# Kernel optimization log

Measured on AMD Instinct MI355X. Metric: run time of the kernel, lower is better.

The kernel has to match this reference:

```python
import jax, jax.numpy as jnp
import numpy as np

N_HEAD = 16


def setup_inputs() -> dict:
    key = jax.random.key(0)
    ks = jax.random.split(key, 5)
    B, T, C = 4, 2048, 1024
    s = 0.02
    x = jax.random.normal(ks[0], (B, T, C), jnp.float32)
    wq = jax.random.normal(ks[1], (C, C), jnp.float32) * s
    wk = jax.random.normal(ks[2], (C, C), jnp.float32) * s
    wv = jax.random.normal(ks[3], (C, C), jnp.float32) * s
    wp = jax.random.normal(ks[4], (C, C), jnp.float32) * s
    zb = jnp.zeros((C,), jnp.float32)
    return {"x": x, "wq": wq, "bq": zb, "wk": wk, "bk": zb,
            "wv": wv, "bv": zb, "wp": wp, "bp": zb}


def _rope_cos_sin(T, D):
    half = D // 2
    i = jnp.arange(half, dtype=jnp.float32)
    alpha = 1.0 / (10000.0 ** (2.0 * i / D))        # [half]
    ang = jnp.arange(T, dtype=jnp.float32)[:, None] * alpha  # [T, half]
    return jnp.cos(ang), jnp.sin(ang)


def _apply_rope(t, cos, sin):
    # t: [B, H, T, D]; non-interleaved halves as in the torch module
    half = t.shape[-1] // 2
    xr, xi = t[..., :half], t[..., half:]
    return jnp.concatenate([xr * cos - xi * sin, xr * sin + xi * cos], axis=-1)


def reference(x, wq, bq, wk, bk, wv, bv, wp, bp):
    B, T, C = x.shape
    H = N_HEAD
    D = C // H
    # QKV projections (torch Linear: x @ W.T + b)
    def heads(w, b):
        return (x @ w.T + b).reshape(B, T, H, D).transpose(0, 2, 1, 3)
    q, k, v = heads(wq, bq), heads(wk, bk), heads(wv, bv)
    cos, sin = _rope_cos_sin(T, D)  # each [T, D//2], broadcasts over B,H
    q = _apply_rope(q, cos, sin)
    k = _apply_rope(k, cos, sin)
    scale = 1.0 / np.sqrt(D).astype(np.float32)
    att = jnp.einsum('bhtd,bhsd->bhts', q, k) * scale  # [B,H,T,T]
    causal = jnp.tril(jnp.ones((T, T), bool))
    att = jnp.where(causal, att, jnp.float32(-jnp.inf))
    att = jax.nn.softmax(att, axis=-1)
    y = jnp.einsum('bhts,bhsd->bhtd', att, v)  # [B,H,T,D]
    y = y.transpose(0, 2, 1, 3).reshape(B, T, C)
    return y @ wp.T + bp
```

## Files before the change

### kernel.cpp

```cpp
#include <hip/hip_runtime.h>
#include <math.h>

constexpr int B = 4, T = 2048, C = 1024, H = 16, D = 64;
constexpr int M = B * T;
constexpr size_t BTC = (size_t)B * T * C;
constexpr float QSCALE = 0.18033688011112042f;
constexpr float ROPE_C = -0.415241011861f;

typedef short bf16x8 __attribute__((ext_vector_type(8)));
typedef float f32x4 __attribute__((ext_vector_type(4)));

__device__ inline ushort f2bf(float f) {
  union { float f; unsigned u; } cv; cv.f = f;
  unsigned u = cv.u;
  u += 0x7fffu + ((u >> 16) & 1u);
  return (ushort)(u >> 16);
}
__device__ inline ushort f2bfr(float f) {
  union { float f; unsigned u; } cv; cv.f = f;
  return (ushort)((cv.u + 0x8000u) >> 16);
}

__device__ inline void async_load16(const void* g, void* l) {
  __builtin_amdgcn_global_load_lds(
      (const __attribute__((address_space(1))) void*)g,
      (__attribute__((address_space(3))) void*)l, 16, 0, 0);
}

__device__ __forceinline__ bf16x8 ones_frag() {
  bf16x8 v;
#pragma unroll
  for (int i = 0; i < 8; i++) v[i] = (short)0x3F80;
  return v;
}

__global__ __launch_bounds__(256) void f32_to_bf16(
    const float* __restrict__ in, ushort* __restrict__ outp) {
  int i = (blockIdx.x * 256 + threadIdx.x) * 4;
  float4 v = *(const float4*)(in + i);
  ushort4 o;
  o.x = f2bf(v.x); o.y = f2bf(v.y); o.z = f2bf(v.z); o.w = f2bf(v.w);
  *(ushort4*)(outp + i) = o;
}

__global__ __launch_bounds__(256) void conv_weights(
    const float* __restrict__ w0, const float* __restrict__ w1,
    const float* __restrict__ w2, const float* __restrict__ w3,
    ushort* __restrict__ outp) {
  const int seg_blocks = (C * C) / 1024;
  int seg = blockIdx.x / seg_blocks;
  int blk = blockIdx.x - seg * seg_blocks;
  const float* src = (seg == 0) ? w0 : (seg == 1) ? w1 : (seg == 2) ? w2 : w3;
  int i = (blk * 256 + threadIdx.x) * 4;
  float4 v = *(const float4*)(src + i);
  ushort4 o;
  o.x = f2bf(v.x); o.y = f2bf(v.y); o.z = f2bf(v.z); o.w = f2bf(v.w);
  *(ushort4*)(outp + (size_t)seg * C * C + i) = o;
}

constexpr int QNT = C / 64;

__global__ __launch_bounds__(512, 2) void gemm_qkv_256x128(
    const ushort* __restrict__ A, const ushort* __restrict__ Wt,
    const float* __restrict__ b0, const float* __restrict__ b1,
    const float* __restrict__ b2, ushort* __restrict__ outq,
    ushort* __restrict__ outk, ushort* __restrict__ outv) {
  __shared__ ushort As[2][256 * 64] __attribute__((aligned(16)));
  __shared__ ushort Bs[3][128 * 64] __attribute__((aligned(16)));
  const int tid = threadIdx.x;
  const int lane = tid & 63;
  const int lrow = lane & 15, quad = lane >> 4;
  const int wave = tid >> 6;
  const int wr = wave >> 1, wc = wave & 1;
  const int x7 = lrow & 7;

  int bid = blockIdx.y * 24 + blockIdx.x;
  int lin = (bid & 7) * 96 + (bid >> 3);
  int row0 = (lin / 24) * 256;
  int col0 = (lin % 24) * 128;

  unsigned gaA[4], gaB[2];
#pragma unroll
  for (int i = 0; i < 4; i++) {
    int c = tid + i * 512;
    int r = c >> 3, cl = c & 7;
    gaA[i] = (unsigned)(row0 + r) * C + (cl ^ (r & 7)) * 8;
  }
#pragma unroll
  for (int i = 0; i < 2; i++) {
    int c = tid + i * 512;
    int r = c >> 3, cl = c & 7;
    gaB[i] = (unsigned)(col0 + r) * C + (cl ^ (r & 7)) * 8;
  }

  f32x4 acc[4][4];
#pragma unroll
  for (int i = 0; i < 4; i++)
#pragma unroll
    for (int j = 0; j < 4; j++) acc[i][j] = (f32x4){0.f, 0.f, 0.f, 0.f};

#pragma unroll
  for (int i = 0; i < 4; i++)
    async_load16(A + gaA[i], &As[0][(tid + i * 512) * 8]);
#pragma unroll
  for (int i = 0; i < 2; i++)
    async_load16(Wt + gaB[i], &Bs[0][(tid + i * 512) * 8]);
#pragma unroll
  for (int i = 0; i < 2; i++)
    async_load16(Wt + gaB[i] + 64, &Bs[1][(tid + i * 512) * 8]);
  asm volatile("s_waitcnt vmcnt(2)" ::: "memory");
  __builtin_amdgcn_sched_barrier(0);
  __builtin_amdgcn_s_barrier();

  int bi = 0;
  for (int t = 0; t < QNT; ++t) {
    const int pa = t & 1;
    const ushort* Ap = As[pa];
    const ushort* Bp = Bs[bi];

    {
      const int slot = (quad ^ x7) * 8;
      bf16x8 af[4], bfr[4];
#pragma unroll
      for (int i = 0; i < 4; i++)
        af[i] = *(const bf16x8*)&Ap[(wr * 64 + i * 16 + lrow) * 64 + slot];
#pragma unroll
      for (int j = 0; j < 4; j++)
        bfr[j] = *(const bf16x8*)&Bp[(wc * 64 + j * 16 + lrow) * 64 + slot];
      if (t + 1 < QNT) {
#pragma unroll
        for (int i = 0; i < 4; i++)
          async_load16(A + gaA[i] + (t + 1) * 64,
                       &As[pa ^ 1][(tid + i * 512) * 8]);
      }
      __builtin_amdgcn_s_barrier();
      asm volatile("s_waitcnt lgkmcnt(0)" ::: "memory");
      __builtin_amdgcn_sched_barrier(0);
      __builtin_amdgcn_s_setprio(1);
#pragma unroll
      for (int i = 0; i < 4; i++)
#pragma unroll
        for (int j = 0; j < 4; j++)
          acc[i][j] = __builtin_amdgcn_mfma_f32_16x16x32_bf16(
              af[i], bfr[j], acc[i][j], 0, 0, 0);
      __builtin_amdgcn_s_setprio(0);
      __builtin_amdgcn_s_barrier();
    }

    {
      const int slot = ((4 + quad) ^ x7) * 8;
      bf16x8 af[4], bfr[4];
#pragma unroll
      for (int i = 0; i < 4; i++)
        af[i] = *(const bf16x8*)&Ap[(wr * 64 + i * 16 + lrow) * 64 + slot];
#pragma unroll
      for (int j = 0; j < 4; j++)
        bfr[j] = *(const bf16x8*)&Bp[(wc * 64 + j * 16 + lrow) * 64 + slot];
      if (t + 2 < QNT) {
        int bi2 = bi - 1; if (bi2 < 0) bi2 = 2;
#pragma unroll
        for (int i = 0; i < 2; i++)
          async_load16(Wt + gaB[i] + (t + 2) * 64,
                       &Bs[bi2][(tid + i * 512) * 8]);
      }
      __builtin_amdgcn_s_barrier();
      asm volatile("s_waitcnt lgkmcnt(0)" ::: "memory");
      __builtin_amdgcn_sched_barrier(0);
      __builtin_amdgcn_s_setprio(1);
#pragma unroll
      for (int i = 0; i < 4; i++)
#pragma unroll
        for (int j = 0; j < 4; j++)
          acc[i][j] = __builtin_amdgcn_mfma_f32_16x16x32_bf16(
              af[i], bfr[j], acc[i][j], 0, 0, 0);
      __builtin_amdgcn_s_setprio(0);
      if (t + 2 < QNT) {
        asm volatile("s_waitcnt vmcnt(2)" ::: "memory");
      } else {
        asm volatile("s_waitcnt vmcnt(0)" ::: "memory");
      }
      __builtin_amdgcn_sched_barrier(0);
      __builtin_amdgcn_s_barrier();
    }
    bi = (bi + 1 == 3) ? 0 : bi + 1;
  }

  const int nb = col0 + wc * 64;
  const int mbase = row0 + wr * 64;
  const float* bias = (col0 < 1024) ? b0 : (col0 < 2048) ? b1 : b2;
  float bn[4];
#pragma unroll
  for (int j = 0; j < 4; j++) bn[j] = bias[(nb & 1023) + j * 16 + lrow];

  int seg = nb >> 10;
  int hh = (nb & 1023) >> 6;
  if (seg < 2) {
    ushort* dst = (seg == 0) ? outq : outk;
    float scale = (seg == 0) ? QSCALE : 1.0f;
    float a0 = __builtin_amdgcn_exp2f((float)lrow * ROPE_C);
    float a1 = __builtin_amdgcn_exp2f((float)(lrow + 16) * ROPE_C);
#pragma unroll
    for (int i = 0; i < 4; i++) {
#pragma unroll
      for (int r = 0; r < 4; r++) {
        int m = mbase + i * 16 + quad * 4 + r;
        int tt = m & (T - 1), bb = m >> 11;
        float s0, c0, s1, c1;
        __sincosf((float)tt * a0, &s0, &c0);
        __sincosf((float)tt * a1, &s1, &c1);
        float xr0 = acc[i][0][r] + bn[0];
        float xi0 = acc[i][2][r] + bn[2];
        float xr1 = acc[i][1][r] + bn[1];
        float xi1 = acc[i][3][r] + bn[3];
        ushort* pp = dst + ((size_t)(bb * H + hh) * T + tt) * D + lrow;
        pp[0]  = f2bf((xr0 * c0 - xi0 * s0) * scale);
        pp[32] = f2bf((xr0 * s0 + xi0 * c0) * scale);
        pp[16] = f2bf((xr1 * c1 - xi1 * s1) * scale);
        pp[48] = f2bf((xr1 * s1 + xi1 * c1) * scale);
      }
    }
  } else {
#pragma unroll
    for (int i = 0; i < 4; i++) {
      int m0 = mbase + i * 16 + quad * 4;
      int t0 = m0 & (T - 1), bb = m0 >> 11;
      size_t base = (size_t)(bb * H + hh) * D * T + t0;
#pragma unroll
      for (int j = 0; j < 4; j++) {
        int d = j * 16 + lrow;
        ushort4 pk;
        pk.x = f2bf(acc[i][j][0] + bn[j]);
        pk.y = f2bf(acc[i][j][1] + bn[j]);
        pk.z = f2bf(acc[i][j][2] + bn[j]);
        pk.w = f2bf(acc[i][j][3] + bn[j]);
        *(ushort4*)(outv + base + (size_t)d * T) = pk;
      }
    }
  }
}

#define GT 128
#define GBK 64
template <int OM>
__global__ __launch_bounds__(256) void gemm_mfma_bt(
    const ushort* __restrict__ A, const ushort* __restrict__ Wt,
    const float* __restrict__ b0, const float* __restrict__ b1,
    const float* __restrict__ b2, void* __restrict__ out1,
    void* __restrict__ out2, void* __restrict__ out3,
    int N, int K) {
  __shared__ ushort As[GT * GBK] __attribute__((aligned(16)));
  __shared__ ushort Bs[GT * GBK] __attribute__((aligned(16)));
  int tid = threadIdx.x;
  int lane = tid & 63;
  int lrow = lane & 15, quad = lane >> 4;
  int wave = tid >> 6;
  int wr = wave >> 1, wc = wave & 1;
  int row0 = blockIdx.y * GT;
  int col0 = blockIdx.x * GT;
  const float* bias = (col0 < 1024) ? b0 : (col0 < 2048) ? b1 : b2;

  size_t ga[4], gb[4];
#pragma unroll
  for (int i = 0; i < 4; i++) {
    int cc = tid + i * 256;
    int r = cc >> 3, cl = cc & 7;
    int g = (cl ^ (r & 7)) * 8;
    ga[i] = (size_t)(row0 + r) * K + g;
    gb[i] = (size_t)(col0 + r) * K + g;
  }
  int x7 = lrow & 7;

  f32x4 acc[4][4];
#pragma unroll
  for (int i = 0; i < 4; i++)
#pragma unroll
    for (int j = 0; j < 4; j++) acc[i][j] = (f32x4){0.f, 0.f, 0.f, 0.f};

  for (int k0 = 0; k0 < K; k0 += GBK) {
#pragma unroll
    for (int i = 0; i < 4; i++) {
      int cc = tid + i * 256;
      async_load16(A + ga[i] + k0, &As[cc * 8]);
      async_load16(Wt + gb[i] + k0, &Bs[cc * 8]);
    }
    __syncthreads();
#pragma unroll
    for (int kh = 0; kh < 2; kh++) {
      int slot = ((kh * 4 + quad) ^ x7) * 8;
      bf16x8 af[4], bfr[4];
#pragma unroll
      for (int i = 0; i < 4; i++)
        af[i] = *(const bf16x8*)&As[(wr * 64 + i * 16 + lrow) * GBK + slot];
#pragma unroll
      for (int j = 0; j < 4; j++)
        bfr[j] = *(const bf16x8*)&Bs[(wc * 64 + j * 16 + lrow) * GBK + slot];
#pragma unroll
      for (int i = 0; i < 4; i++)
#pragma unroll
        for (int j = 0; j < 4; j++)
          acc[i][j] = __builtin_amdgcn_mfma_f32_16x16x32_bf16(af[i], bfr[j], acc[i][j], 0, 0, 0);
    }
    __syncthreads();
  }

  int nb = col0 + wc * 64;
  int mbase = row0 + wr * 64;
  float bn[4];
#pragma unroll
  for (int j = 0; j < 4; j++) bn[j] = bias[(nb & 1023) + j * 16 + lrow];

  if (OM == 0) {
    float* outp = (float*)out1;
#pragma unroll
    for (int i = 0; i < 4; i++)
#pragma unroll
      for (int j = 0; j < 4; j++) {
        int n = nb + j * 16 + lrow;
#pragma unroll
        for (int r = 0; r < 4; r++) {
          int m = mbase + i * 16 + quad * 4 + r;
          outp[(size_t)m * N + n] = acc[i][j][r] + bn[j];
        }
      }
  }
}

__device__ __forceinline__ void stage_kv(
    const ushort* kbh, const ushort* vbh, int s0,
    ushort* Kl, ushort* Vl, int tid) {
#pragma unroll
  for (int i = 0; i < 2; i++) {
    int c = tid + i * 256;
    int r = c >> 3, cc = c & 7;
    int g = (cc ^ (r & 7)) * 8;
    async_load16(kbh + (size_t)(s0 + r) * D + g, Kl + c * 8);
    async_load16(vbh + (size_t)r * T + s0 + g, Vl + c * 8);
  }
}

template <int MODE>
__device__ __forceinline__ void attn_step4(
    int s0, const ushort* KL, const ushort* VL, ushort* P,
    const bf16x8 (&qf)[2][2], int lrow, int quad, int sw0, int sw1,
    int qg0, int qg1, f32x4 (&o)[4][2], f32x4 (&ol)[2]) {
  bf16x8 kf0[4], kf1[4];
#pragma unroll
  for (int kt = 0; kt < 4; kt++) {
    int base = (kt * 16 + lrow) * 64;
    kf0[kt] = *(const bf16x8*)&KL[base + sw0];
    kf1[kt] = *(const bf16x8*)&KL[base + sw1];
  }
  bf16x8 vf0[4], vf1[4];
#pragma unroll
  for (int ds = 0; ds < 4; ds++) {
    int base = (ds * 16 + lrow) * 64;
    vf0[ds] = *(const bf16x8*)&VL[base + sw0];
    vf1[ds] = *(const bf16x8*)&VL[base + sw1];
  }
#pragma unroll
  for (int g = 0; g < 2; g++) {
    if (MODE == 2 && g == 0) continue;
    int qg = g ? qg1 : qg0;
    f32x4 st[4];
#pragma unroll
    for (int kt = 0; kt < 4; kt++) {
      f32x4 z = {0.f, 0.f, 0.f, 0.f};
      st[kt] = __builtin_amdgcn_mfma_f32_16x16x32_bf16(kf0[kt], qf[g][0], z, 0, 0, 0);
      st[kt] = __builtin_amdgcn_mfma_f32_16x16x32_bf16(kf1[kt], qf[g][1], st[kt], 0, 0, 0);
    }
    if ((MODE == 1 && g == 0) || (MODE == 2 && g == 1)) {
#pragma unroll
      for (int kt = 0; kt < 4; kt++)
#pragma unroll
        for (int r = 0; r < 4; r++)
          if (s0 + kt * 16 + quad * 4 + r > qg) st[kt][r] = -1e30f;
    }
#pragma unroll
    for (int kt = 0; kt < 4; kt++) {
      ushort4 pk;
      pk.x = f2bfr(__builtin_amdgcn_exp2f(st[kt][0]));
      pk.y = f2bfr(__builtin_amdgcn_exp2f(st[kt][1]));
      pk.z = f2bfr(__builtin_amdgcn_exp2f(st[kt][2]));
      pk.w = f2bfr(__builtin_amdgcn_exp2f(st[kt][3]));
      *(ushort4*)&P[((2 * kt + (quad >> 1)) * 32 + g * 16 + lrow) * 8 + (quad & 1) * 4] = pk;
    }
  }
  asm volatile("" ::: "memory");
  bf16x8 ones = ones_frag();
#pragma unroll
  for (int g = 0; g < 2; g++) {
    if (MODE == 2 && g == 0) continue;
    bf16x8 pf0 = *(const bf16x8*)&P[(quad * 32 + g * 16 + lrow) * 8];
    bf16x8 pf1 = *(const bf16x8*)&P[((quad + 4) * 32 + g * 16 + lrow) * 8];
    ol[g] = __builtin_amdgcn_mfma_f32_16x16x32_bf16(ones, pf0, ol[g], 0, 0, 0);
    ol[g] = __builtin_amdgcn_mfma_f32_16x16x32_bf16(ones, pf1, ol[g], 0, 0, 0);
#pragma unroll
    for (int ds = 0; ds < 4; ds++) {
      o[ds][g] = __builtin_amdgcn_mfma_f32_16x16x32_bf16(vf0[ds], pf0, o[ds][g], 0, 0, 0);
      o[ds][g] = __builtin_amdgcn_mfma_f32_16x16x32_bf16(vf1[ds], pf1, o[ds][g], 0, 0, 0);
    }
  }
}

__global__ __launch_bounds__(256, 3) void attn_mfma4(
    const ushort* __restrict__ qb_, const ushort* __restrict__ kb_,
    const ushort* __restrict__ vtb_, ushort* __restrict__ y) {
  __shared__ ushort Kl[2][64 * 64] __attribute__((aligned(16)));
  __shared__ ushort Vl[2][64 * 64] __attribute__((aligned(16)));
  __shared__ ushort Pl[4][2048] __attribute__((aligned(16)));
  int tid = threadIdx.x;
  int wave = tid >> 6, lane = tid & 63;
  int lrow = lane & 15, quad = lane >> 4;
  int qbi = 15 - (int)(blockIdx.x >> 6);
  int bh = blockIdx.x & 63;
  int b = bh >> 4, h = bh & 15;
  int Q0 = qbi * 128;
  ushort* P = Pl[wave];
  const ushort* kbh = kb_ + (size_t)bh * T * D;
  const ushort* vbh = vtb_ + (size_t)bh * D * T;

  int qg0 = Q0 + wave * 16 + lrow;
  int qg1 = qg0 + 64;
  bf16x8 qf[2][2];
  {
    const ushort* qp0 = qb_ + ((size_t)bh * T + qg0) * D + quad * 8;
    qf[0][0] = *(const bf16x8*)qp0;
    qf[0][1] = *(const bf16x8*)(qp0 + 32);
    const ushort* qp1 = qb_ + ((size_t)bh * T + qg1) * D + quad * 8;
    qf[1][0] = *(const bf16x8*)qp1;
    qf[1][1] = *(const bf16x8*)(qp1 + 32);
  }
  int r7 = lrow & 7;
  int sw0 = (quad ^ r7) * 8;
  int sw1 = ((quad + 4) ^ r7) * 8;

  f32x4 o[4][2];
#pragma unroll
  for (int ds = 0; ds < 4; ds++)
#pragma unroll
    for (int g = 0; g < 2; g++) o[ds][g] = (f32x4){0.f, 0.f, 0.f, 0.f};
  f32x4 ol[2] = {(f32x4){0.f, 0.f, 0.f, 0.f}, (f32x4){0.f, 0.f, 0.f, 0.f}};

  int trips = 2 * qbi + 2;
  stage_kv(kbh, vbh, 0, Kl[0], Vl[0], tid);
  int it = 0;
  for (; it < trips - 2; ++it) {
    __syncthreads();
    stage_kv(kbh, vbh, (it + 1) * 64, Kl[(it + 1) & 1], Vl[(it + 1) & 1], tid);
    attn_step4<0>(it * 64, Kl[it & 1], Vl[it & 1], P, qf, lrow, quad, sw0, sw1,
                  qg0, qg1, o, ol);
  }
  __syncthreads();
  stage_kv(kbh, vbh, (it + 1) * 64, Kl[(it + 1) & 1], Vl[(it + 1) & 1], tid);
  attn_step4<1>(it * 64, Kl[it & 1], Vl[it & 1], P, qf, lrow, quad, sw0, sw1,
                qg0, qg1, o, ol);
  ++it;
  __syncthreads();
  attn_step4<2>(it * 64, Kl[it & 1], Vl[it & 1], P, qf, lrow, quad, sw0, sw1,
                qg0, qg1, o, ol);

#pragma unroll
  for (int g = 0; g < 2; g++) {
    float inv = 1.f / ol[g][0];
    int qg = g ? qg1 : qg0;
#pragma unroll
    for (int ds = 0; ds < 4; ds++) {
      ushort4 pk;
      pk.x = f2bf(o[ds][g][0] * inv);
      pk.y = f2bf(o[ds][g][1] * inv);
      pk.z = f2bf(o[ds][g][2] * inv);
      pk.w = f2bf(o[ds][g][3] * inv);
      *(ushort4*)(y + ((size_t)b * T + qg) * C + h * D + ds * 16 + quad * 4) = pk;
    }
  }
}

extern "C" void kernel_launch(void* const* d_in, const int* in_sizes, int n_in,
                              void* d_out, int out_size, void* d_ws, size_t ws_size,
                              hipStream_t stream) {
  const float* x  = (const float*)d_in[0];
  const float* wq = (const float*)d_in[1];
  const float* bq = (const float*)d_in[2];
  const float* wk = (const float*)d_in[3];
  const float* bk = (const float*)d_in[4];
  const float* wv = (const float*)d_in[5];
  const float* bv = (const float*)d_in[6];
  const float* wp = (const float*)d_in[7];
  const float* bp = (const float*)d_in[8];
  float* out = (float*)d_out;

  ushort* xb    = (ushort*)d_ws;
  ushort* qb    = xb + BTC;
  ushort* kb    = qb + BTC;
  ushort* vtb   = kb + BTC;
  ushort* yb    = vtb + BTC;
  ushort* wqkvb = yb + BTC;
  ushort* wpb   = wqkvb + (size_t)3 * C * C;

  f32_to_bf16<<<(int)(BTC / 1024), 256, 0, stream>>>(x, xb);
  conv_weights<<<4 * (C * C) / 1024, 256, 0, stream>>>(wq, wk, wv, wp, wqkvb);

  dim3 qkv_grid(3 * C / 128, M / 256);
  gemm_qkv_256x128<<<qkv_grid, 512, 0, stream>>>(
      xb, wqkvb, bq, bk, bv, qb, kb, vtb);

  attn_mfma4<<<(B * H * T / 128), 256, 0, stream>>>(qb, kb, vtb, yb);

  dim3 proj_grid(C / GT, M / GT);
  gemm_mfma_bt<0><<<proj_grid, 256, 0, stream>>>(
      yb, wpb, bp, bp, bp, out, nullptr, nullptr, C, C);
}
```

Before: 247.2 us.

## Generalize pipelined 256x128 GEMM, use it for projection, drop intra-step barriers

Turns the triple-buffered, software-pipelined QKV GEMM into a template that takes an output mode and a column-tile count. The output projection now uses it in place of the simpler 128x128 kernel, which synchronised twice per K step and had no load/compute overlap. The main loop also drops the per-half barriers and explicit lgkmcnt waits, keeping a single vmcnt wait plus barrier per K iteration. This is meant to cut barrier stalls and hide global-load latency in both GEMMs. In exchange it relies on the single end-of-iteration barrier and compiler-inserted LDS waits for correctness, and the projection launch now uses larger 512-thread tiles, so there are fewer blocks.

Measured after the change: 231.5 us. -6.4%, faster.

```diff
diff --git a/kernel.cpp b/kernel.cpp
--- a/kernel.cpp
+++ b/kernel.cpp
@@ -60,11 +60,12 @@
 
 constexpr int QNT = C / 64;
 
-__global__ __launch_bounds__(512, 2) void gemm_qkv_256x128(
+template <int OM, int NCT>
+__global__ __launch_bounds__(512, 2) void gemm_pipe(
     const ushort* __restrict__ A, const ushort* __restrict__ Wt,
     const float* __restrict__ b0, const float* __restrict__ b1,
-    const float* __restrict__ b2, ushort* __restrict__ outq,
-    ushort* __restrict__ outk, ushort* __restrict__ outv) {
+    const float* __restrict__ b2, void* __restrict__ out1,
+    void* __restrict__ out2, void* __restrict__ out3) {
   __shared__ ushort As[2][256 * 64] __attribute__((aligned(16)));
   __shared__ ushort Bs[3][128 * 64] __attribute__((aligned(16)));
   const int tid = threadIdx.x;
@@ -74,10 +75,11 @@
   const int wr = wave >> 1, wc = wave & 1;
   const int x7 = lrow & 7;
 
-  int bid = blockIdx.y * 24 + blockIdx.x;
-  int lin = (bid & 7) * 96 + (bid >> 3);
-  int row0 = (lin / 24) * 256;
-  int col0 = (lin % 24) * 128;
+  int bid = blockIdx.y * NCT + blockIdx.x;
+  const int cpx = NCT * 4;
+  int lin = (bid & 7) * cpx + (bid >> 3);
+  int row0 = (lin / NCT) * 256;
+  int col0 = (lin % NCT) * 128;
 
   unsigned gaA[4], gaB[2];
 #pragma unroll
@@ -117,72 +119,66 @@
     const int pa = t & 1;
     const ushort* Ap = As[pa];
     const ushort* Bp = Bs[bi];
+    int bi2 = bi - 1; if (bi2 < 0) bi2 = 2;
 
     {
       const int slot = (quad ^ x7) * 8;
-      bf16x8 af[4], bfr[4];
+      bf16x8 aF[4], bF[4];
 #pragma unroll
       for (int i = 0; i < 4; i++)
-        af[i] = *(const bf16x8*)&Ap[(wr * 64 + i * 16 + lrow) * 64 + slot];
+        aF[i] = *(const bf16x8*)&Ap[(wr * 64 + i * 16 + lrow) * 64 + slot];
 #pragma unroll
       for (int j = 0; j < 4; j++)
-        bfr[j] = *(const bf16x8*)&Bp[(wc * 64 + j * 16 + lrow) * 64 + slot];
+        bF[j] = *(const bf16x8*)&Bp[(wc * 64 + j * 16 + lrow) * 64 + slot];
       if (t + 1 < QNT) {
 #pragma unroll
         for (int i = 0; i < 4; i++)
           async_load16(A + gaA[i] + (t + 1) * 64,
                        &As[pa ^ 1][(tid + i * 512) * 8]);
       }
-      __builtin_amdgcn_s_barrier();
-      asm volatile("s_waitcnt lgkmcnt(0)" ::: "memory");
-      __builtin_amdgcn_sched_barrier(0);
       __builtin_amdgcn_s_setprio(1);
 #pragma unroll
       for (int i = 0; i < 4; i++)
 #pragma unroll
         for (int j = 0; j < 4; j++)
           acc[i][j] = __builtin_amdgcn_mfma_f32_16x16x32_bf16(
-              af[i], bfr[j], acc[i][j], 0, 0, 0);
+              aF[i], bF[j], acc[i][j], 0, 0, 0);
       __builtin_amdgcn_s_setprio(0);
-      __builtin_amdgcn_s_barrier();
     }
 
     {
       const int slot = ((4 + quad) ^ x7) * 8;
-      bf16x8 af[4], bfr[4];
+      bf16x8 aF[4], bF[4];
 #pragma unroll
       for (int i = 0; i < 4; i++)
-        af[i] = *(const bf16x8*)&Ap[(wr * 64 + i * 16 + lrow) * 64 + slot];
+        aF[i] = *(const bf16x8*)&Ap[(wr * 64 + i * 16 + lrow) * 64 + slot];
 #pragma unroll
       for (int j = 0; j < 4; j++)
-        bfr[j] = *(const bf16x8*)&Bp[(wc * 64 + j * 16 + lrow) * 64 + slot];
+        bF[j] = *(const bf16x8*)&Bp[(wc * 64 + j * 16 + lrow) * 64 + slot];
       if (t + 2 < QNT) {
-        int bi2 = bi - 1; if (bi2 < 0) bi2 = 2;
 #pragma unroll
         for (int i = 0; i < 2; i++)
           async_load16(Wt + gaB[i] + (t + 2) * 64,
                        &Bs[bi2][(tid + i * 512) * 8]);
       }
-      __builtin_amdgcn_s_barrier();
-      asm volatile("s_waitcnt lgkmcnt(0)" ::: "memory");
-      __builtin_amdgcn_sched_barrier(0);
       __builtin_amdgcn_s_setprio(1);
 #pragma unroll
       for (int i = 0; i < 4; i++)
 #pragma unroll
         for (int j = 0; j < 4; j++)
           acc[i][j] = __builtin_amdgcn_mfma_f32_16x16x32_bf16(
-              af[i], bfr[j], acc[i][j], 0, 0, 0);
+              aF[i], bF[j], acc[i][j], 0, 0, 0);
       __builtin_amdgcn_s_setprio(0);
-      if (t + 2 < QNT) {
-        asm volatile("s_waitcnt vmcnt(2)" ::: "memory");
-      } else {
-        asm volatile("s_waitcnt vmcnt(0)" ::: "memory");
-      }
-      __builtin_amdgcn_sched_barrier(0);
-      __builtin_amdgcn_s_barrier();
-    }
-    bi = (bi + 1 == 3) ? 0 : bi + 1;
+    }
+
+    if (t + 2 < QNT) {
+      asm volatile("s_waitcnt vmcnt(2)" ::: "memory");
+    } else {
+      asm volatile("s_waitcnt vmcnt(0)" ::: "memory");
+    }
+    __builtin_amdgcn_sched_barrier(0);
+    __builtin_amdgcn_s_barrier();
+    bi = (bi == 2) ? 0 : bi + 1;
   }
 
   const int nb = col0 + wc * 64;
@@ -192,124 +188,8 @@
 #pragma unroll
   for (int j = 0; j < 4; j++) bn[j] = bias[(nb & 1023) + j * 16 + lrow];
 
-  int seg = nb >> 10;
-  int hh = (nb & 1023) >> 6;
-  if (seg < 2) {
-    ushort* dst = (seg == 0) ? outq : outk;
-    float scale = (seg == 0) ? QSCALE : 1.0f;
-    float a0 = __builtin_amdgcn_exp2f((float)lrow * ROPE_C);
-    float a1 = __builtin_amdgcn_exp2f((float)(lrow + 16) * ROPE_C);
-#pragma unroll
-    for (int i = 0; i < 4; i++) {
-#pragma unroll
-      for (int r = 0; r < 4; r++) {
-        int m = mbase + i * 16 + quad * 4 + r;
-        int tt = m & (T - 1), bb = m >> 11;
-        float s0, c0, s1, c1;
-        __sincosf((float)tt * a0, &s0, &c0);
-        __sincosf((float)tt * a1, &s1, &c1);
-        float xr0 = acc[i][0][r] + bn[0];
-        float xi0 = acc[i][2][r] + bn[2];
-        float xr1 = acc[i][1][r] + bn[1];
-        float xi1 = acc[i][3][r] + bn[3];
-        ushort* pp = dst + ((size_t)(bb * H + hh) * T + tt) * D + lrow;
-        pp[0]  = f2bf((xr0 * c0 - xi0 * s0) * scale);
-        pp[32] = f2bf((xr0 * s0 + xi0 * c0) * scale);
-        pp[16] = f2bf((xr1 * c1 - xi1 * s1) * scale);
-        pp[48] = f2bf((xr1 * s1 + xi1 * c1) * scale);
-      }
-    }
-  } else {
-#pragma unroll
-    for (int i = 0; i < 4; i++) {
-      int m0 = mbase + i * 16 + quad * 4;
-      int t0 = m0 & (T - 1), bb = m0 >> 11;
-      size_t base = (size_t)(bb * H + hh) * D * T + t0;
-#pragma unroll
-      for (int j = 0; j < 4; j++) {
-        int d = j * 16 + lrow;
-        ushort4 pk;
-        pk.x = f2bf(acc[i][j][0] + bn[j]);
-        pk.y = f2bf(acc[i][j][1] + bn[j]);
-        pk.z = f2bf(acc[i][j][2] + bn[j]);
-        pk.w = f2bf(acc[i][j][3] + bn[j]);
-        *(ushort4*)(outv + base + (size_t)d * T) = pk;
-      }
-    }
-  }
-}
-
-#define GT 128
-#define GBK 64
-template <int OM>
-__global__ __launch_bounds__(256) void gemm_mfma_bt(
-    const ushort* __restrict__ A, const ushort* __restrict__ Wt,
-    const float* __restrict__ b0, const float* __restrict__ b1,
-    const float* __restrict__ b2, void* __restrict__ out1,
-    void* __restrict__ out2, void* __restrict__ out3,
-    int N, int K) {
-  __shared__ ushort As[GT * GBK] __attribute__((aligned(16)));
-  __shared__ ushort Bs[GT * GBK] __attribute__((aligned(16)));
-  int tid = threadIdx.x;
-  int lane = tid & 63;
-  int lrow = lane & 15, quad = lane >> 4;
-  int wave = tid >> 6;
-  int wr = wave >> 1, wc = wave & 1;
-  int row0 = blockIdx.y * GT;
-  int col0 = blockIdx.x * GT;
-  const float* bias = (col0 < 1024) ? b0 : (col0 < 2048) ? b1 : b2;
-
-  size_t ga[4], gb[4];
-#pragma unroll
-  for (int i = 0; i < 4; i++) {
-    int cc = tid + i * 256;
-    int r = cc >> 3, cl = cc & 7;
-    int g = (cl ^ (r & 7)) * 8;
-    ga[i] = (size_t)(row0 + r) * K + g;
-    gb[i] = (size_t)(col0 + r) * K + g;
-  }
-  int x7 = lrow & 7;
-
-  f32x4 acc[4][4];
-#pragma unroll
-  for (int i = 0; i < 4; i++)
-#pragma unroll
-    for (int j = 0; j < 4; j++) acc[i][j] = (f32x4){0.f, 0.f, 0.f, 0.f};
-
-  for (int k0 = 0; k0 < K; k0 += GBK) {
-#pragma unroll
-    for (int i = 0; i < 4; i++) {
-      int cc = tid + i * 256;
-      async_load16(A + ga[i] + k0, &As[cc * 8]);
-      async_load16(Wt + gb[i] + k0, &Bs[cc * 8]);
-    }
-    __syncthreads();
-#pragma unroll
-    for (int kh = 0; kh < 2; kh++) {
-      int slot = ((kh * 4 + quad) ^ x7) * 8;
-      bf16x8 af[4], bfr[4];
-#pragma unroll
-      for (int i = 0; i < 4; i++)
-        af[i] = *(const bf16x8*)&As[(wr * 64 + i * 16 + lrow) * GBK + slot];
-#pragma unroll
-      for (int j = 0; j < 4; j++)
-        bfr[j] = *(const bf16x8*)&Bs[(wc * 64 + j * 16 + lrow) * GBK + slot];
-#pragma unroll
-      for (int i = 0; i < 4; i++)
-#pragma unroll
-        for (int j = 0; j < 4; j++)
-          acc[i][j] = __builtin_amdgcn_mfma_f32_16x16x32_bf16(af[i], bfr[j], acc[i][j], 0, 0, 0);
-    }
-    __syncthreads();
-  }
-
-  int nb = col0 + wc * 64;
-  int mbase = row0 + wr * 64;
-  float bn[4];
-#pragma unroll
-  for (int j = 0; j < 4; j++) bn[j] = bias[(nb & 1023) + j * 16 + lrow];
-
   if (OM == 0) {
+    const int N = NCT * 128;
     float* outp = (float*)out1;
 #pragma unroll
     for (int i = 0; i < 4; i++)
@@ -322,6 +202,53 @@
           outp[(size_t)m * N + n] = acc[i][j][r] + bn[j];
         }
       }
+  } else {
+    int seg = nb >> 10;
+    int hh = (nb & 1023) >> 6;
+    if (seg < 2) {
+      ushort* dst = (seg == 0) ? (ushort*)out1 : (ushort*)out2;
+      float scale = (seg == 0) ? QSCALE : 1.0f;
+      float a0 = __builtin_amdgcn_exp2f((float)lrow * ROPE_C);
+      float a1 = __builtin_amdgcn_exp2f((float)(lrow + 16) * ROPE_C);
+#pragma unroll
+      for (int i = 0; i < 4; i++) {
+#pragma unroll
+        for (int r = 0; r < 4; r++) {
+          int m = mbase + i * 16 + quad * 4 + r;
+          int tt = m & (T - 1), bb = m >> 11;
+          float s0, c0, s1, c1;
+          __sincosf((float)tt * a0, &s0, &c0);
+          __sincosf((float)tt * a1, &s1, &c1);
+          float xr0 = acc[i][0][r] + bn[0];
+          float xi0 = acc[i][2][r] + bn[2];
+          float xr1 = acc[i][1][r] + bn[1];
+          float xi1 = acc[i][3][r] + bn[3];
+          ushort* pp = dst + ((size_t)(bb * H + hh) * T + tt) * D + lrow;
+          pp[0]  = f2bf((xr0 * c0 - xi0 * s0) * scale);
+          pp[32] = f2bf((xr0 * s0 + xi0 * c0) * scale);
+          pp[16] = f2bf((xr1 * c1 - xi1 * s1) * scale);
+          pp[48] = f2bf((xr1 * s1 + xi1 * c1) * scale);
+        }
+      }
+    } else {
+      ushort* dst = (ushort*)out3;
+#pragma unroll
+      for (int i = 0; i < 4; i++) {
+        int m0 = mbase + i * 16 + quad * 4;
+        int t0 = m0 & (T - 1), bb = m0 >> 11;
+        size_t base = (size_t)(bb * H + hh) * D * T + t0;
+#pragma unroll
+        for (int j = 0; j < 4; j++) {
+          int d = j * 16 + lrow;
+          ushort4 pk;
+          pk.x = f2bf(acc[i][j][0] + bn[j]);
+          pk.y = f2bf(acc[i][j][1] + bn[j]);
+          pk.z = f2bf(acc[i][j][2] + bn[j]);
+          pk.w = f2bf(acc[i][j][3] + bn[j]);
+          *(ushort4*)(dst + base + (size_t)d * T) = pk;
+        }
+      }
+    }
   }
 }
 
@@ -501,12 +428,12 @@
   conv_weights<<<4 * (C * C) / 1024, 256, 0, stream>>>(wq, wk, wv, wp, wqkvb);
 
   dim3 qkv_grid(3 * C / 128, M / 256);
-  gemm_qkv_256x128<<<qkv_grid, 512, 0, stream>>>(
+  gemm_pipe<1, 24><<<qkv_grid, 512, 0, stream>>>(
       xb, wqkvb, bq, bk, bv, qb, kb, vtb);
 
   attn_mfma4<<<(B * H * T / 128), 256, 0, stream>>>(qb, kb, vtb, yb);
 
-  dim3 proj_grid(C / GT, M / GT);
-  gemm_mfma_bt<0><<<proj_grid, 256, 0, stream>>>(
-      yb, wpb, bp, bp, bp, out, nullptr, nullptr, C, C);
-}
+  dim3 proj_grid(C / 128, M / 256);
+  gemm_pipe<0, 8><<<proj_grid, 512, 0, stream>>>(
+      yb, wpb, bp, bp, bp, out, nullptr, nullptr);
+}
```
